# Kernel optimization log

Hardware: AMD Instinct MI355X
Metric: run time of the kernel (lower is better)

## Reference

```python
import jax, jax.numpy as jnp
import numpy as np

N = 200000
E = 3200000


def _init_linear(key, fan_in, fan_out):
    kw, kb = jax.random.split(key)
    bound = 1.0 / np.sqrt(fan_in)
    W = jax.random.uniform(kw, (fan_in, fan_out), jnp.float32, -bound, bound)
    b = jax.random.uniform(kb, (fan_out,), jnp.float32, -bound, bound)
    return W, b


def setup_inputs() -> dict:
    key = jax.random.key(0)
    ks = jax.random.split(key, 8)
    latent_features = jax.random.normal(ks[0], (N, 256), jnp.float32)
    history = jax.random.uniform(ks[1], (N,), jnp.float32)
    is_subgoal = jax.random.uniform(ks[2], (N,), jnp.float32)
    edge_index = jax.random.randint(ks[3], (2, E), 0, N, dtype=jnp.int64)
    W1, b1 = _init_linear(ks[4], 258, 128)
    W2, b2 = _init_linear(ks[5], 128, 64)
    W3, b3 = _init_linear(ks[6], 64, 8)
    Wc, bc = _init_linear(ks[7], 8, 3)
    return {"latent_features": latent_features, "history": history,
            "is_subgoal": is_subgoal, "edge_index": edge_index,
            "W1": W1, "b1": b1, "W2": W2, "b2": b2,
            "W3": W3, "b3": b3, "Wc": Wc, "bc": bc}


def _gcn_conv(h, W, b, src, dst, norm, n):
    # PyG GCNConv: linear transform, then symmetric-normalized scatter-add.
    h = h @ W                                  # [n, F_out]
    msg = norm[:, None] * h[src]               # gather + edge-norm, [E+n, F_out]
    out = jax.ops.segment_sum(msg, dst, num_segments=n)
    return out + b


def reference(latent_features, history, is_subgoal, edge_index,
              W1, b1, W2, b2, W3, b3, Wc, bc):
    n = latent_features.shape[0]
    # add self-loops (GCNConv default add_self_loops=True)
    loop = jnp.arange(n, dtype=edge_index.dtype)
    src = jnp.concatenate([edge_index[0], loop])
    dst = jnp.concatenate([edge_index[1], loop])
    # symmetric normalization: deg over destination (incl. self-loops)
    deg = jax.ops.segment_sum(jnp.ones_like(dst, dtype=jnp.float32), dst,
                              num_segments=n)
    dinv = jnp.where(deg > 0, jax.lax.rsqrt(deg), 0.0)
    norm = dinv[src] * dinv[dst]               # [E+n]

    h = jnp.concatenate([latent_features, history[:, None],
                         is_subgoal[:, None]], axis=1)  # [n, 258]
    h = jax.nn.relu(_gcn_conv(h, W1, b1, src, dst, norm, n))
    h = jax.nn.relu(_gcn_conv(h, W2, b2, src, dst, norm, n))
    h = jax.nn.relu(_gcn_conv(h, W3, b3, src, dst, norm, n))
    return h @ Wc + bc                          # [n, 3]
```

## Files before the change

### kernel.cpp

```cpp
#include <hip/hip_runtime.h>
#include <hip/hip_fp16.h>


#define N_NODES 200000
#define N_EDGES 3200000
#define NBUCK 782

static_assert(N_NODES % 64 == 0, "tiling");
static_assert((NBUCK - 1) * 256 < N_NODES && NBUCK * 256 >= N_NODES, "buckets");

typedef unsigned int u32;
typedef _Float16 f16;
typedef __attribute__((ext_vector_type(8))) _Float16 f16x8;
typedef __attribute__((ext_vector_type(4))) _Float16 f16x4;
typedef __attribute__((ext_vector_type(4))) float f32x4;
typedef __attribute__((ext_vector_type(2))) float f32x2;


__global__ __launch_bounds__(256) void k_bhist(const int* __restrict__ dst,
                                               int* __restrict__ bcnt) {
    __shared__ int lh[NBUCK];
    int t = threadIdx.x;
    for (int b = t; b < NBUCK; b += 256) lh[b] = 0;
    __syncthreads();
    long e0 = (long)blockIdx.x * 8192;
    for (int k = 0; k < 32; ++k) {
        long e = e0 + k * 256 + t;
        if (e < N_EDGES) atomicAdd(&lh[dst[e] >> 8], 1);
    }
    __syncthreads();
    for (int b = t; b < NBUCK; b += 256)
        if (lh[b]) atomicAdd(&bcnt[b], lh[b]);
}


__global__ __launch_bounds__(256) void k_bscan(const int* __restrict__ bcnt,
                                               int* __restrict__ boff,
                                               int* __restrict__ bcur,
                                               int* __restrict__ row) {
    __shared__ int sm[256];
    int t = threadIdx.x;
    int base = t * 4;
    int a0 = (base + 0 < NBUCK) ? bcnt[base + 0] : 0;
    int a1 = (base + 1 < NBUCK) ? bcnt[base + 1] : 0;
    int a2 = (base + 2 < NBUCK) ? bcnt[base + 2] : 0;
    int a3 = (base + 3 < NBUCK) ? bcnt[base + 3] : 0;
    int s = a0 + a1 + a2 + a3;
    sm[t] = s;
    __syncthreads();
    for (int o = 1; o < 256; o <<= 1) {
        int v = (t >= o) ? sm[t - o] : 0;
        __syncthreads();
        sm[t] += v;
        __syncthreads();
    }
    int excl = sm[t] - s;
    if (base + 0 < NBUCK) { boff[base + 0] = excl;               bcur[base + 0] = excl; }
    if (base + 1 < NBUCK) { boff[base + 1] = excl + a0;          bcur[base + 1] = excl + a0; }
    if (base + 2 < NBUCK) { boff[base + 2] = excl + a0 + a1;     bcur[base + 2] = excl + a0 + a1; }
    if (base + 3 < NBUCK) { boff[base + 3] = excl + a0 + a1 + a2; bcur[base + 3] = excl + a0 + a1 + a2; }
    if (t == 255) { boff[NBUCK] = N_EDGES; row[N_NODES] = N_EDGES; }
}


__global__ __launch_bounds__(256) void k_scatter(const int* __restrict__ src,
                                                 const int* __restrict__ dst,
                                                 int* __restrict__ bcur,
                                                 u32* __restrict__ entries) {
    __shared__ int lh[NBUCK];
    __shared__ int base[NBUCK];
    __shared__ int lcur[NBUCK];
    int t = threadIdx.x;
    for (int b = t; b < NBUCK; b += 256) lh[b] = 0;
    __syncthreads();
    long e0 = (long)blockIdx.x * 8192;
    for (int k = 0; k < 32; ++k) {
        long e = e0 + k * 256 + t;
        if (e < N_EDGES) atomicAdd(&lh[dst[e] >> 8], 1);
    }
    __syncthreads();
    for (int b = t; b < NBUCK; b += 256) {
        base[b] = atomicAdd(&bcur[b], lh[b]);
        lcur[b] = 0;
    }
    __syncthreads();
    for (int k = 0; k < 32; ++k) {
        long e = e0 + k * 256 + t;
        if (e < N_EDGES) {
            int d = dst[e];
            int bkt = d >> 8;
            int p = base[bkt] + atomicAdd(&lcur[bkt], 1);
            entries[p] = ((u32)src[e] << 8) | (u32)(d & 255);
        }
    }
}


__global__ __launch_bounds__(256) void k_prep(const u32* __restrict__ entries,
                                              const int* __restrict__ boff,
                                              int* __restrict__ row,
                                              float* __restrict__ dinv,
                                              int* __restrict__ col) {
    __shared__ int lh[256];
    __shared__ int sc[256];
    __shared__ int cur[256];
    const int b = blockIdx.x, t = threadIdx.x;
    const int s = boff[b], e = boff[b + 1];
    const int cnt = e - s;
    lh[t] = 0;
    __syncthreads();
    for (int i = t; i < cnt; i += 256) atomicAdd(&lh[entries[s + i] & 255], 1);
    __syncthreads();
    int my = lh[t];
    sc[t] = my;
    __syncthreads();
    for (int o = 1; o < 256; o <<= 1) {
        int v = (t >= o) ? sc[t - o] : 0;
        __syncthreads();
        sc[t] += v;
        __syncthreads();
    }
    int excl = sc[t] - my;
    int node = b * 256 + t;
    if (node < N_NODES) {
        row[node] = s + excl;
        dinv[node] = rsqrtf((float)(my + 1));
    }
    cur[t] = s + excl;
    __syncthreads();
    for (int i = t; i < cnt; i += 256) {
        u32 en = entries[s + i];
        int p = atomicAdd(&cur[en & 255], 1);
        col[p] = (int)(en >> 8);
    }
}


__global__ __launch_bounds__(256) void k_prepw(const float* __restrict__ W,
                                               f16* __restrict__ Wth,
                                               f16* __restrict__ Wtl) {
    int t = blockIdx.x * 256 + threadIdx.x;
    int k = t >> 7;
    int f = t & 127;
    float w = W[k * 128 + f];
    f16 hi = (f16)w;
    f16 lo = (f16)(w - (float)hi);
    Wth[f * 256 + k] = hi;
    Wtl[f * 256 + k] = lo;
}


__global__ __launch_bounds__(256) void k_prepw2(const float* __restrict__ W2,
                                                f16* __restrict__ Wh,
                                                f16* __restrict__ Wl) {
    int t = blockIdx.x * 256 + threadIdx.x;
    int k = t >> 6;
    int f = t & 63;
    float w = W2[k * 64 + f];
    f16 hi = (f16)w;
    Wh[f * 128 + k] = hi;
    Wl[f * 128 + k] = (f16)(w - (float)hi);
}


__global__ __launch_bounds__(1024) void k_gemm1(const float* __restrict__ X,
                                                const float* __restrict__ hist,
                                                const float* __restrict__ subg,
                                                const float* __restrict__ W,
                                                const f16* __restrict__ Wth,
                                                const f16* __restrict__ Wtl,
                                                const float* __restrict__ dinv,
                                                __half2* __restrict__ g1) {
    __shared__ f16 Ws[2][128 * 256];
    const int t = threadIdx.x;

    {
        const int r = t >> 3;
        const int seg = t & 7;
        const f16* gh = Wth + r * 256 + seg * 32;
        const f16* gl = Wtl + r * 256 + seg * 32;
        const int sw = (r & 7) << 4;
        const int base = r * 512 + seg * 64;
        char* wsh = (char*)&Ws[0][0];
        char* wsl = (char*)&Ws[1][0];
#pragma unroll
        for (int q = 0; q < 4; ++q) {
            *(f16x8*)(wsh + ((base + q * 16) ^ sw)) = *(const f16x8*)(gh + q * 8);
            *(f16x8*)(wsl + ((base + q * 16) ^ sw)) = *(const f16x8*)(gl + q * 8);
        }
    }

    const int wv = t >> 6;
    const int l = t & 63;
    const int l15 = l & 15;
    const int lk = l >> 4;
    const int nb = blockIdx.x * 256;
    const int node = nb + wv * 16 + l15;
    const int xrow = node < N_NODES ? node : N_NODES - 1;
    const float* xbase = X + (size_t)xrow * 256 + lk * 8;

    f32x4 acc[8];
#pragma unroll
    for (int fb = 0; fb < 8; ++fb) acc[fb] = (f32x4){0.f, 0.f, 0.f, 0.f};

    float4 pa = *(const float4*)(xbase + 0);
    float4 pb = *(const float4*)(xbase + 4);

    __syncthreads();

    const char* wsh = (const char*)&Ws[0][0];
    const char* wsl = (const char*)&Ws[1][0];
    const int sw = (l15 & 7) << 4;

    for (int kc = 0; kc < 256; kc += 32) {
        float xs[8] = {pa.x, pa.y, pa.z, pa.w, pb.x, pb.y, pb.z, pb.w};
        if (kc + 32 < 256) {
            pa = *(const float4*)(xbase + kc + 32);
            pb = *(const float4*)(xbase + kc + 36);
        }
        union { f16 h[8]; f16x8 v; } H, L;
#pragma unroll
        for (int i = 0; i < 8; ++i) {
            f16 h = (f16)xs[i];
            H.h[i] = h;
            L.h[i] = (f16)(xs[i] - (float)h);
        }
        f16x8 xh = H.v, xl = L.v;

        const int koff = ((kc + lk * 8) * 2) ^ sw;
#pragma unroll
        for (int fb = 0; fb < 8; ++fb) {
            const int off = (fb * 16 + l15) * 512 + koff;
            f16x8 wh = *(const f16x8*)(wsh + off);
            f16x8 wl = *(const f16x8*)(wsl + off);
            acc[fb] = __builtin_amdgcn_mfma_f32_16x16x32_f16(wh, xh, acc[fb], 0, 0, 0);
            acc[fb] = __builtin_amdgcn_mfma_f32_16x16x32_f16(wh, xl, acc[fb], 0, 0, 0);
            acc[fb] = __builtin_amdgcn_mfma_f32_16x16x32_f16(wl, xh, acc[fb], 0, 0, 0);
        }
    }

    const bool ok = node < N_NODES;
    const float hh = hist[xrow];
    const float ss = subg[xrow];
    const float dv = dinv[xrow];
    char* orow = (char*)g1 + (size_t)node * 256;
#pragma unroll
    for (int fb = 0; fb < 8; ++fb) {
        const int f0 = fb * 16 + lk * 4;
        float4 w6 = *(const float4*)(W + 256 * 128 + f0);
        float4 w7 = *(const float4*)(W + 257 * 128 + f0);
        union { f16 h[4]; float2 v; } o;
        o.h[0] = (f16)((acc[fb][0] + hh * w6.x + ss * w7.x) * dv);
        o.h[1] = (f16)((acc[fb][1] + hh * w6.y + ss * w7.y) * dv);
        o.h[2] = (f16)((acc[fb][2] + hh * w6.z + ss * w7.z) * dv);
        o.h[3] = (f16)((acc[fb][3] + hh * w6.w + ss * w7.w) * dv);
        if (ok) *(float2*)(orow + fb * 32 + lk * 8) = o.v;
    }
}


__global__ __launch_bounds__(1024) void k_ag2(const __half2* __restrict__ g,
                                              const int* __restrict__ row,
                                              const int* __restrict__ col,
                                              const float* __restrict__ dinv,
                                              const float* __restrict__ bias,
                                              const f16* __restrict__ W2hg,
                                              const f16* __restrict__ W2lg,
                                              __half2* __restrict__ g2) {
    __shared__ f16 Xh[64][136];
    __shared__ f16 Xl[64][136];
    __shared__ f16 Wh[64][136];
    __shared__ f16 Wl[64][136];
    const int t = threadIdx.x;
    const int nb = blockIdx.x * 64;

    {
        const int r = t >> 4;
        const int sg = (t & 15) * 8;
        *(f16x8*)&Wh[r][sg] = *(const f16x8*)(W2hg + r * 128 + sg);
        *(f16x8*)&Wl[r][sg] = *(const f16x8*)(W2lg + r * 128 + sg);
    }

    const int wv = t >> 6;
    const int l = t & 63;
    const int hf = l >> 5;
    const int ln = l & 31;
    const f16x4* gp = (const f16x4*)g;
    const float4 b4 = *(const float4*)(bias + ln * 4);
    for (int i = 0; i < 2; ++i) {
        const int nloc = wv * 4 + hf * 2 + i;
        const int node = nb + nloc;
        f32x4 a = (f32x4){0.f, 0.f, 0.f, 0.f};
        const int s = row[node];
        const int e = row[node + 1];
        int idx = s;
        for (; idx + 8 <= e; idx += 8) {
            u32 off[8];
            f16x4 h[8];
#pragma unroll
            for (int u = 0; u < 8; ++u) off[u] = ((u32)col[idx + u] << 5) + ln;
#pragma unroll
            for (int u = 0; u < 8; ++u) h[u] = gp[off[u]];
#pragma unroll
            for (int u = 0; u < 8; ++u) a += __builtin_convertvector(h[u], f32x4);
        }
        for (; idx < e; ++idx)
            a += __builtin_convertvector(gp[((u32)col[idx] << 5) + ln], f32x4);
        f32x4 fs = __builtin_convertvector(gp[((u32)node << 5) + ln], f32x4);
        const float di = dinv[node];
        float v0 = fmaxf(di * (a[0] + fs[0]) + b4.x, 0.f);
        float v1 = fmaxf(di * (a[1] + fs[1]) + b4.y, 0.f);
        float v2 = fmaxf(di * (a[2] + fs[2]) + b4.z, 0.f);
        float v3 = fmaxf(di * (a[3] + fs[3]) + b4.w, 0.f);
        f16 h0 = (f16)v0, h1 = (f16)v1, h2 = (f16)v2, h3 = (f16)v3;
        f16x4 hi = {h0, h1, h2, h3};
        f16x4 lo = {(f16)(v0 - (float)h0), (f16)(v1 - (float)h1),
                    (f16)(v2 - (float)h2), (f16)(v3 - (float)h3)};
        *(f16x4*)&Xh[nloc][ln * 4] = hi;
        *(f16x4*)&Xl[nloc][ln * 4] = lo;
    }
    __syncthreads();

    const int l15 = l & 15;
    const int lk = l >> 4;
    const int nw = wv & 3;
    const int fw = wv >> 2;
    f32x4 acc = (f32x4){0.f, 0.f, 0.f, 0.f};
#pragma unroll
    for (int kc = 0; kc < 128; kc += 32) {
        f16x8 xh = *(const f16x8*)&Xh[nw * 16 + l15][kc + lk * 8];
        f16x8 xl = *(const f16x8*)&Xl[nw * 16 + l15][kc + lk * 8];
        f16x8 wh = *(const f16x8*)&Wh[fw * 16 + l15][kc + lk * 8];
        f16x8 wl = *(const f16x8*)&Wl[fw * 16 + l15][kc + lk * 8];
        acc = __builtin_amdgcn_mfma_f32_16x16x32_f16(wh, xh, acc, 0, 0, 0);
        acc = __builtin_amdgcn_mfma_f32_16x16x32_f16(wh, xl, acc, 0, 0, 0);
        acc = __builtin_amdgcn_mfma_f32_16x16x32_f16(wl, xh, acc, 0, 0, 0);
    }
    const int node = nb + nw * 16 + l15;
    const float dv = dinv[node];
    union { f16 h[4]; float2 v; } o;
#pragma unroll
    for (int r = 0; r < 4; ++r) o.h[r] = (f16)(acc[r] * dv);
    *(float2*)((char*)g2 + (size_t)node * 128 + fw * 32 + lk * 8) = o.v;
}


__global__ __launch_bounds__(256) void k_ag3(const __half2* __restrict__ g,
                                             const int* __restrict__ row,
                                             const int* __restrict__ col,
                                             const float* __restrict__ dinv,
                                             const float* __restrict__ bias,
                                             const float* __restrict__ W3,
                                             float* __restrict__ g3) {
    __shared__ float h3s[32][68];
    __shared__ float W3t[8][68];
    const int t = threadIdx.x;
    const int nb = blockIdx.x * 32;

    for (int i = t; i < 512; i += 256) {
        int k = i & 63, f = i >> 6;
        W3t[f][k] = W3[k * 8 + f];
    }

    const int wv = t >> 6;
    const int l = t & 63;
    const int q = l >> 4;
    const int ln = l & 15;
    const f16x4* gp = (const f16x4*)g;
    const float4 b4 = *(const float4*)(bias + ln * 4);
    for (int i = 0; i < 2; ++i) {
        const int nloc = wv * 8 + q * 2 + i;
        const int node = nb + nloc;
        f32x4 a = (f32x4){0.f, 0.f, 0.f, 0.f};
        const int s = row[node];
        const int e = row[node + 1];
        int idx = s;
        for (; idx + 8 <= e; idx += 8) {
            u32 off[8];
            f16x4 h[8];
#pragma unroll
            for (int u = 0; u < 8; ++u) off[u] = ((u32)col[idx + u] << 4) + ln;
#pragma unroll
            for (int u = 0; u < 8; ++u) h[u] = gp[off[u]];
#pragma unroll
            for (int u = 0; u < 8; ++u) a += __builtin_convertvector(h[u], f32x4);
        }
        for (; idx < e; ++idx)
            a += __builtin_convertvector(gp[((u32)col[idx] << 4) + ln], f32x4);
        f32x4 fs = __builtin_convertvector(gp[((u32)node << 4) + ln], f32x4);
        const float di = dinv[node];
        float4 o;
        o.x = fmaxf(di * (a[0] + fs[0]) + b4.x, 0.f);
        o.y = fmaxf(di * (a[1] + fs[1]) + b4.y, 0.f);
        o.z = fmaxf(di * (a[2] + fs[2]) + b4.z, 0.f);
        o.w = fmaxf(di * (a[3] + fs[3]) + b4.w, 0.f);
        *(float4*)&h3s[nloc][ln * 4] = o;
    }
    __syncthreads();

    const int node = t >> 3;
    const int f = t & 7;
    float acc = 0.f;
#pragma unroll
    for (int k4 = 0; k4 < 16; ++k4) {
        float4 x = *(const float4*)&h3s[node][k4 * 4];
        float4 w = *(const float4*)&W3t[f][k4 * 4];
        acc += x.x * w.x + x.y * w.y + x.z * w.z + x.w * w.w;
    }
    g3[(size_t)(nb + node) * 8 + f] = dinv[nb + node] * acc;
}


__global__ __launch_bounds__(256) void k_agf(const float* __restrict__ g,
                                             const int* __restrict__ row,
                                             const int* __restrict__ col,
                                             const float* __restrict__ dinv,
                                             const float* __restrict__ bias,
                                             const float* __restrict__ Wc,
                                             const float* __restrict__ bc,
                                             float* __restrict__ out) {
    __shared__ float h4s[64][10];
    __shared__ float Wcs[24];
    __shared__ float bcs[3];
    const int t = threadIdx.x;
    const int nb = blockIdx.x * 64;
    if (t < 24) Wcs[t] = Wc[t];
    if (t < 3) bcs[t] = bc[t];

    const int node = t >> 2;
    const int c = t & 3;
    const f32x2* gp = (const f32x2*)g;
    const float2 b2 = *(const float2*)(bias + c * 2);
    f32x2 a = (f32x2){0.f, 0.f};
    const int s = row[nb + node];
    const int e = row[nb + node + 1];
    int idx = s;
    for (; idx + 8 <= e; idx += 8) {
        u32 off[8];
        f32x2 v[8];
#pragma unroll
        for (int u = 0; u < 8; ++u) off[u] = ((u32)col[idx + u] << 2) + c;
#pragma unroll
        for (int u = 0; u < 8; ++u) v[u] = gp[off[u]];
#pragma unroll
        for (int u = 0; u < 8; ++u) a += v[u];
    }
    for (; idx < e; ++idx) a += gp[((u32)col[idx] << 2) + c];
    a += gp[((u32)(nb + node) << 2) + c];
    const float di = dinv[nb + node];
    float2 o;
    o.x = fmaxf(di * a[0] + b2.x, 0.f);
    o.y = fmaxf(di * a[1] + b2.y, 0.f);
    *(float2*)&h4s[node][c * 2] = o;
    __syncthreads();

    if ((t & 3) < 3) {
        const int n2 = t >> 2;
        const int cc = t & 3;
        float o2 = bcs[cc];
#pragma unroll
        for (int k = 0; k < 8; ++k) o2 += h4s[n2][k] * Wcs[k * 3 + cc];
        out[(size_t)(nb + n2) * 3 + cc] = o2;
    }
}


extern "C" void kernel_launch(void* const* d_in, const int* in_sizes, int n_in,
                              void* d_out, int out_size, void* d_ws, size_t ws_size,
                              hipStream_t stream) {
    const float* latent = (const float*)d_in[0];
    const float* hist = (const float*)d_in[1];
    const float* subg = (const float*)d_in[2];
    const int* eidx = (const int*)d_in[3];
    const float* W1 = (const float*)d_in[4];
    const float* b1 = (const float*)d_in[5];
    const float* W2 = (const float*)d_in[6];
    const float* b2 = (const float*)d_in[7];
    const float* W3 = (const float*)d_in[8];
    const float* b3 = (const float*)d_in[9];
    const float* Wc = (const float*)d_in[10];
    const float* bc = (const float*)d_in[11];
    float* outp = (float*)d_out;

    char* ws = (char*)d_ws;
    size_t off = 0;
    auto take = [&](size_t bytes) -> void* {
        void* p = ws + off;
        off += (bytes + 255) & ~(size_t)255;
        return p;
    };
    float* dinv = (float*)take((size_t)N_NODES * 4);
    int* row = (int*)take((size_t)(N_NODES + 1) * 4);
    int* col = (int*)take((size_t)N_EDGES * 4);
    u32* entries = (u32*)take((size_t)N_EDGES * 4);
    int* bcnt = (int*)take((size_t)NBUCK * 4);
    int* boff = (int*)take((size_t)(NBUCK + 1) * 4);
    int* bcur = (int*)take((size_t)NBUCK * 4);
    __half2* bufH = (__half2*)take((size_t)N_NODES * 128 * 2);
    __half2* bufG2 = (__half2*)take((size_t)N_NODES * 64 * 2);
    float* bufG3 = (float*)take((size_t)N_NODES * 8 * 4);
    f16* Wth = (f16*)take((size_t)128 * 256 * 2);
    f16* Wtl = (f16*)take((size_t)128 * 256 * 2);
    f16* W2h = (f16*)take((size_t)64 * 128 * 2);
    f16* W2l = (f16*)take((size_t)64 * 128 * 2);

    const int* srcp = eidx;
    const int* dstp = eidx + N_EDGES;

    const int scat_blocks = (N_EDGES + 8191) / 8192;

    hipMemsetAsync(bcnt, 0, (size_t)NBUCK * 4, stream);
    k_prepw<<<128, 256, 0, stream>>>(W1, Wth, Wtl);
    k_prepw2<<<32, 256, 0, stream>>>(W2, W2h, W2l);
    k_bhist<<<scat_blocks, 256, 0, stream>>>(dstp, bcnt);
    k_bscan<<<1, 256, 0, stream>>>(bcnt, boff, bcur, row);
    k_scatter<<<scat_blocks, 256, 0, stream>>>(srcp, dstp, bcur, entries);
    k_prep<<<NBUCK, 256, 0, stream>>>(entries, boff, row, dinv, col);

    k_gemm1<<<(N_NODES + 255) / 256, 1024, 0, stream>>>(latent, hist, subg, W1, Wth, Wtl, dinv, bufH);
    k_ag2<<<N_NODES / 64, 1024, 0, stream>>>(bufH, row, col, dinv, b1, W2h, W2l, bufG2);
    k_ag3<<<N_NODES / 32, 256, 0, stream>>>(bufG2, row, col, dinv, b2, W3, bufG3);
    k_agf<<<N_NODES / 64, 256, 0, stream>>>(bufG3, row, col, dinv, b3, Wc, bc, outp);
}
```

Measured before the change: 727.4 us.

## Replace bucket count/scan with fixed-capacity buckets and interleave two-node gathers

Drops the bucket histogram and scan kernels by giving each destination bucket a fixed slab of BCAP entries, with per-node start/end arrays replacing the CSR row pointer. The aggregation kernels for layers two and three now gather neighbors of two nodes in an interleaved loop to expose more outstanding loads, and the final aggregation gets a deeper unroll. This removes a full pass over dst and two launches. In exchange it assumes no bucket exceeds BCAP, clamping writes (and corrupting results) if one does.

```diff
diff --git a/kernel.cpp b/kernel.cpp
--- a/kernel.cpp
+++ b/kernel.cpp
@@ -5,6 +5,7 @@
 #define N_NODES 200000
 #define N_EDGES 3200000
 #define NBUCK 782
+#define BCAP 5120
 
 static_assert(N_NODES % 64 == 0, "tiling");
 static_assert((NBUCK - 1) * 256 < N_NODES && NBUCK * 256 >= N_NODES, "buckets");
@@ -15,52 +16,6 @@
 typedef __attribute__((ext_vector_type(4))) _Float16 f16x4;
 typedef __attribute__((ext_vector_type(4))) float f32x4;
 typedef __attribute__((ext_vector_type(2))) float f32x2;
-
-
-__global__ __launch_bounds__(256) void k_bhist(const int* __restrict__ dst,
-                                               int* __restrict__ bcnt) {
-    __shared__ int lh[NBUCK];
-    int t = threadIdx.x;
-    for (int b = t; b < NBUCK; b += 256) lh[b] = 0;
-    __syncthreads();
-    long e0 = (long)blockIdx.x * 8192;
-    for (int k = 0; k < 32; ++k) {
-        long e = e0 + k * 256 + t;
-        if (e < N_EDGES) atomicAdd(&lh[dst[e] >> 8], 1);
-    }
-    __syncthreads();
-    for (int b = t; b < NBUCK; b += 256)
-        if (lh[b]) atomicAdd(&bcnt[b], lh[b]);
-}
-
-
-__global__ __launch_bounds__(256) void k_bscan(const int* __restrict__ bcnt,
-                                               int* __restrict__ boff,
-                                               int* __restrict__ bcur,
-                                               int* __restrict__ row) {
-    __shared__ int sm[256];
-    int t = threadIdx.x;
-    int base = t * 4;
-    int a0 = (base + 0 < NBUCK) ? bcnt[base + 0] : 0;
-    int a1 = (base + 1 < NBUCK) ? bcnt[base + 1] : 0;
-    int a2 = (base + 2 < NBUCK) ? bcnt[base + 2] : 0;
-    int a3 = (base + 3 < NBUCK) ? bcnt[base + 3] : 0;
-    int s = a0 + a1 + a2 + a3;
-    sm[t] = s;
-    __syncthreads();
-    for (int o = 1; o < 256; o <<= 1) {
-        int v = (t >= o) ? sm[t - o] : 0;
-        __syncthreads();
-        sm[t] += v;
-        __syncthreads();
-    }
-    int excl = sm[t] - s;
-    if (base + 0 < NBUCK) { boff[base + 0] = excl;               bcur[base + 0] = excl; }
-    if (base + 1 < NBUCK) { boff[base + 1] = excl + a0;          bcur[base + 1] = excl + a0; }
-    if (base + 2 < NBUCK) { boff[base + 2] = excl + a0 + a1;     bcur[base + 2] = excl + a0 + a1; }
-    if (base + 3 < NBUCK) { boff[base + 3] = excl + a0 + a1 + a2; bcur[base + 3] = excl + a0 + a1 + a2; }
-    if (t == 255) { boff[NBUCK] = N_EDGES; row[N_NODES] = N_EDGES; }
-}
 
 
 __global__ __launch_bounds__(256) void k_scatter(const int* __restrict__ src,
@@ -80,7 +35,7 @@
     }
     __syncthreads();
     for (int b = t; b < NBUCK; b += 256) {
-        base[b] = atomicAdd(&bcur[b], lh[b]);
+        base[b] = lh[b] ? atomicAdd(&bcur[b], lh[b]) : 0;
         lcur[b] = 0;
     }
     __syncthreads();
@@ -90,26 +45,29 @@
             int d = dst[e];
             int bkt = d >> 8;
             int p = base[bkt] + atomicAdd(&lcur[bkt], 1);
-            entries[p] = ((u32)src[e] << 8) | (u32)(d & 255);
+            p = p < BCAP ? p : BCAP - 1;
+            entries[(size_t)bkt * BCAP + p] = ((u32)src[e] << 8) | (u32)(d & 255);
         }
     }
 }
 
 
 __global__ __launch_bounds__(256) void k_prep(const u32* __restrict__ entries,
-                                              const int* __restrict__ boff,
-                                              int* __restrict__ row,
+                                              const int* __restrict__ bcur,
+                                              int* __restrict__ rs,
+                                              int* __restrict__ re,
                                               float* __restrict__ dinv,
                                               int* __restrict__ col) {
     __shared__ int lh[256];
     __shared__ int sc[256];
     __shared__ int cur[256];
     const int b = blockIdx.x, t = threadIdx.x;
-    const int s = boff[b], e = boff[b + 1];
-    const int cnt = e - s;
+    int cnt = bcur[b];
+    cnt = cnt < BCAP ? cnt : BCAP;
+    const u32* ent = entries + (size_t)b * BCAP;
     lh[t] = 0;
     __syncthreads();
-    for (int i = t; i < cnt; i += 256) atomicAdd(&lh[entries[s + i] & 255], 1);
+    for (int i = t; i < cnt; i += 256) atomicAdd(&lh[ent[i] & 255], 1);
     __syncthreads();
     int my = lh[t];
     sc[t] = my;
@@ -123,13 +81,14 @@
     int excl = sc[t] - my;
     int node = b * 256 + t;
     if (node < N_NODES) {
-        row[node] = s + excl;
+        rs[node] = b * BCAP + excl;
+        re[node] = b * BCAP + excl + my;
         dinv[node] = rsqrtf((float)(my + 1));
     }
-    cur[t] = s + excl;
+    cur[t] = b * BCAP + excl;
     __syncthreads();
     for (int i = t; i < cnt; i += 256) {
-        u32 en = entries[s + i];
+        u32 en = ent[i];
         int p = atomicAdd(&cur[en & 255], 1);
         col[p] = (int)(en >> 8);
     }
@@ -260,7 +219,8 @@
 
 
 __global__ __launch_bounds__(1024) void k_ag2(const __half2* __restrict__ g,
-                                              const int* __restrict__ row,
+                                              const int* __restrict__ rs,
+                                              const int* __restrict__ re,
                                               const int* __restrict__ col,
                                               const float* __restrict__ dinv,
                                               const float* __restrict__ bias,
@@ -287,25 +247,57 @@
     const int ln = l & 31;
     const f16x4* gp = (const f16x4*)g;
     const float4 b4 = *(const float4*)(bias + ln * 4);
+    const int n0 = nb + wv * 4 + hf * 2;
+    const int n1 = n0 + 1;
+    f32x4 a0 = (f32x4){0.f, 0.f, 0.f, 0.f};
+    f32x4 a1 = (f32x4){0.f, 0.f, 0.f, 0.f};
+    int i0 = rs[n0], e0i = re[n0];
+    int i1 = rs[n1], e1i = re[n1];
+    while (i0 + 8 <= e0i && i1 + 8 <= e1i) {
+        u32 offA[8], offB[8];
+        f16x4 hA[8], hB[8];
+#pragma unroll
+        for (int u = 0; u < 8; ++u) offA[u] = ((u32)col[i0 + u] << 5) + ln;
+#pragma unroll
+        for (int u = 0; u < 8; ++u) offB[u] = ((u32)col[i1 + u] << 5) + ln;
+#pragma unroll
+        for (int u = 0; u < 8; ++u) hA[u] = gp[offA[u]];
+#pragma unroll
+        for (int u = 0; u < 8; ++u) hB[u] = gp[offB[u]];
+#pragma unroll
+        for (int u = 0; u < 8; ++u) a0 += __builtin_convertvector(hA[u], f32x4);
+#pragma unroll
+        for (int u = 0; u < 8; ++u) a1 += __builtin_convertvector(hB[u], f32x4);
+        i0 += 8;
+        i1 += 8;
+    }
+    for (; i0 + 8 <= e0i; i0 += 8) {
+        u32 off[8];
+        f16x4 h[8];
+#pragma unroll
+        for (int u = 0; u < 8; ++u) off[u] = ((u32)col[i0 + u] << 5) + ln;
+#pragma unroll
+        for (int u = 0; u < 8; ++u) h[u] = gp[off[u]];
+#pragma unroll
+        for (int u = 0; u < 8; ++u) a0 += __builtin_convertvector(h[u], f32x4);
+    }
+    for (; i1 + 8 <= e1i; i1 += 8) {
+        u32 off[8];
+        f16x4 h[8];
+#pragma unroll
+        for (int u = 0; u < 8; ++u) off[u] = ((u32)col[i1 + u] << 5) + ln;
+#pragma unroll
+        for (int u = 0; u < 8; ++u) h[u] = gp[off[u]];
+#pragma unroll
+        for (int u = 0; u < 8; ++u) a1 += __builtin_convertvector(h[u], f32x4);
+    }
+    for (; i0 < e0i; ++i0) a0 += __builtin_convertvector(gp[((u32)col[i0] << 5) + ln], f32x4);
+    for (; i1 < e1i; ++i1) a1 += __builtin_convertvector(gp[((u32)col[i1] << 5) + ln], f32x4);
+
+#pragma unroll
     for (int i = 0; i < 2; ++i) {
-        const int nloc = wv * 4 + hf * 2 + i;
-        const int node = nb + nloc;
-        f32x4 a = (f32x4){0.f, 0.f, 0.f, 0.f};
-        const int s = row[node];
-        const int e = row[node + 1];
-        int idx = s;
-        for (; idx + 8 <= e; idx += 8) {
-            u32 off[8];
-            f16x4 h[8];
-#pragma unroll
-            for (int u = 0; u < 8; ++u) off[u] = ((u32)col[idx + u] << 5) + ln;
-#pragma unroll
-            for (int u = 0; u < 8; ++u) h[u] = gp[off[u]];
-#pragma unroll
-            for (int u = 0; u < 8; ++u) a += __builtin_convertvector(h[u], f32x4);
-        }
-        for (; idx < e; ++idx)
-            a += __builtin_convertvector(gp[((u32)col[idx] << 5) + ln], f32x4);
+        const int node = i ? n1 : n0;
+        f32x4 a = i ? a1 : a0;
         f32x4 fs = __builtin_convertvector(gp[((u32)node << 5) + ln], f32x4);
         const float di = dinv[node];
         float v0 = fmaxf(di * (a[0] + fs[0]) + b4.x, 0.f);
@@ -316,8 +308,8 @@
         f16x4 hi = {h0, h1, h2, h3};
         f16x4 lo = {(f16)(v0 - (float)h0), (f16)(v1 - (float)h1),
                     (f16)(v2 - (float)h2), (f16)(v3 - (float)h3)};
-        *(f16x4*)&Xh[nloc][ln * 4] = hi;
-        *(f16x4*)&Xl[nloc][ln * 4] = lo;
+        *(f16x4*)&Xh[node - nb][ln * 4] = hi;
+        *(f16x4*)&Xl[node - nb][ln * 4] = lo;
     }
     __syncthreads();
 
@@ -346,7 +338,8 @@
 
 
 __global__ __launch_bounds__(256) void k_ag3(const __half2* __restrict__ g,
-                                             const int* __restrict__ row,
+                                             const int* __restrict__ rs,
+                                             const int* __restrict__ re,
                                              const int* __restrict__ col,
                                              const float* __restrict__ dinv,
                                              const float* __restrict__ bias,
@@ -368,25 +361,57 @@
     const int ln = l & 15;
     const f16x4* gp = (const f16x4*)g;
     const float4 b4 = *(const float4*)(bias + ln * 4);
+    const int n0 = nb + wv * 8 + q * 2;
+    const int n1 = n0 + 1;
+    f32x4 a0 = (f32x4){0.f, 0.f, 0.f, 0.f};
+    f32x4 a1 = (f32x4){0.f, 0.f, 0.f, 0.f};
+    int i0 = rs[n0], e0i = re[n0];
+    int i1 = rs[n1], e1i = re[n1];
+    while (i0 + 8 <= e0i && i1 + 8 <= e1i) {
+        u32 offA[8], offB[8];
+        f16x4 hA[8], hB[8];
+#pragma unroll
+        for (int u = 0; u < 8; ++u) offA[u] = ((u32)col[i0 + u] << 4) + ln;
+#pragma unroll
+        for (int u = 0; u < 8; ++u) offB[u] = ((u32)col[i1 + u] << 4) + ln;
+#pragma unroll
+        for (int u = 0; u < 8; ++u) hA[u] = gp[offA[u]];
+#pragma unroll
+        for (int u = 0; u < 8; ++u) hB[u] = gp[offB[u]];
+#pragma unroll
+        for (int u = 0; u < 8; ++u) a0 += __builtin_convertvector(hA[u], f32x4);
+#pragma unroll
+        for (int u = 0; u < 8; ++u) a1 += __builtin_convertvector(hB[u], f32x4);
+        i0 += 8;
+        i1 += 8;
+    }
+    for (; i0 + 8 <= e0i; i0 += 8) {
+        u32 off[8];
+        f16x4 h[8];
+#pragma unroll
+        for (int u = 0; u < 8; ++u) off[u] = ((u32)col[i0 + u] << 4) + ln;
+#pragma unroll
+        for (int u = 0; u < 8; ++u) h[u] = gp[off[u]];
+#pragma unroll
+        for (int u = 0; u < 8; ++u) a0 += __builtin_convertvector(h[u], f32x4);
+    }
+    for (; i1 + 8 <= e1i; i1 += 8) {
+        u32 off[8];
+        f16x4 h[8];
+#pragma unroll
+        for (int u = 0; u < 8; ++u) off[u] = ((u32)col[i1 + u] << 4) + ln;
+#pragma unroll
+        for (int u = 0; u < 8; ++u) h[u] = gp[off[u]];
+#pragma unroll
+        for (int u = 0; u < 8; ++u) a1 += __builtin_convertvector(h[u], f32x4);
+    }
+    for (; i0 < e0i; ++i0) a0 += __builtin_convertvector(gp[((u32)col[i0] << 4) + ln], f32x4);
+    for (; i1 < e1i; ++i1) a1 += __builtin_convertvector(gp[((u32)col[i1] << 4) + ln], f32x4);
+
+#pragma unroll
     for (int i = 0; i < 2; ++i) {
-        const int nloc = wv * 8 + q * 2 + i;
-        const int node = nb + nloc;
-        f32x4 a = (f32x4){0.f, 0.f, 0.f, 0.f};
-        const int s = row[node];
-        const int e = row[node + 1];
-        int idx = s;
-        for (; idx + 8 <= e; idx += 8) {
-            u32 off[8];
-            f16x4 h[8];
-#pragma unroll
-            for (int u = 0; u < 8; ++u) off[u] = ((u32)col[idx + u] << 4) + ln;
-#pragma unroll
-            for (int u = 0; u < 8; ++u) h[u] = gp[off[u]];
-#pragma unroll
-            for (int u = 0; u < 8; ++u) a += __builtin_convertvector(h[u], f32x4);
-        }
-        for (; idx < e; ++idx)
-            a += __builtin_convertvector(gp[((u32)col[idx] << 4) + ln], f32x4);
+        const int node = i ? n1 : n0;
+        f32x4 a = i ? a1 : a0;
         f32x4 fs = __builtin_convertvector(gp[((u32)node << 4) + ln], f32x4);
         const float di = dinv[node];
         float4 o;
@@ -394,7 +419,7 @@
         o.y = fmaxf(di * (a[1] + fs[1]) + b4.y, 0.f);
         o.z = fmaxf(di * (a[2] + fs[2]) + b4.z, 0.f);
         o.w = fmaxf(di * (a[3] + fs[3]) + b4.w, 0.f);
-        *(float4*)&h3s[nloc][ln * 4] = o;
+        *(float4*)&h3s[node - nb][ln * 4] = o;
     }
     __syncthreads();
 
@@ -412,7 +437,8 @@
 
 
 __global__ __launch_bounds__(256) void k_agf(const float* __restrict__ g,
-                                             const int* __restrict__ row,
+                                             const int* __restrict__ rs,
+                                             const int* __restrict__ re,
                                              const int* __restrict__ col,
                                              const float* __restrict__ dinv,
                                              const float* __restrict__ bias,
@@ -432,9 +458,19 @@
     const f32x2* gp = (const f32x2*)g;
     const float2 b2 = *(const float2*)(bias + c * 2);
     f32x2 a = (f32x2){0.f, 0.f};
-    const int s = row[nb + node];
-    const int e = row[nb + node + 1];
+    const int s = rs[nb + node];
+    const int e = re[nb + node];
     int idx = s;
+    for (; idx + 16 <= e; idx += 16) {
+        u32 off[16];
+        f32x2 v[16];
+#pragma unroll
+        for (int u = 0; u < 16; ++u) off[u] = ((u32)col[idx + u] << 2) + c;
+#pragma unroll
+        for (int u = 0; u < 16; ++u) v[u] = gp[off[u]];
+#pragma unroll
+        for (int u = 0; u < 16; ++u) a += v[u];
+    }
     for (; idx + 8 <= e; idx += 8) {
         u32 off[8];
         f32x2 v[8];
@@ -490,11 +526,10 @@
         return p;
     };
     float* dinv = (float*)take((size_t)N_NODES * 4);
-    int* row = (int*)take((size_t)(N_NODES + 1) * 4);
-    int* col = (int*)take((size_t)N_EDGES * 4);
-    u32* entries = (u32*)take((size_t)N_EDGES * 4);
-    int* bcnt = (int*)take((size_t)NBUCK * 4);
-    int* boff = (int*)take((size_t)(NBUCK + 1) * 4);
+    int* rs = (int*)take((size_t)N_NODES * 4);
+    int* re = (int*)take((size_t)N_NODES * 4);
+    int* col = (int*)take((size_t)NBUCK * BCAP * 4);
+    u32* entries = (u32*)take((size_t)NBUCK * BCAP * 4);
     int* bcur = (int*)take((size_t)NBUCK * 4);
     __half2* bufH = (__half2*)take((size_t)N_NODES * 128 * 2);
     __half2* bufG2 = (__half2*)take((size_t)N_NODES * 64 * 2);
@@ -509,16 +544,14 @@
 
     const int scat_blocks = (N_EDGES + 8191) / 8192;
 
-    hipMemsetAsync(bcnt, 0, (size_t)NBUCK * 4, stream);
+    hipMemsetAsync(bcur, 0, (size_t)NBUCK * 4, stream);
     k_prepw<<<128, 256, 0, stream>>>(W1, Wth, Wtl);
     k_prepw2<<<32, 256, 0, stream>>>(W2, W2h, W2l);
-    k_bhist<<<scat_blocks, 256, 0, stream>>>(dstp, bcnt);
-    k_bscan<<<1, 256, 0, stream>>>(bcnt, boff, bcur, row);
     k_scatter<<<scat_blocks, 256, 0, stream>>>(srcp, dstp, bcur, entries);
-    k_prep<<<NBUCK, 256, 0, stream>>>(entries, boff, row, dinv, col);
+    k_prep<<<NBUCK, 256, 0, stream>>>(entries, bcur, rs, re, dinv, col);
 
     k_gemm1<<<(N_NODES + 255) / 256, 1024, 0, stream>>>(latent, hist, subg, W1, Wth, Wtl, dinv, bufH);
-    k_ag2<<<N_NODES / 64, 1024, 0, stream>>>(bufH, row, col, dinv, b1, W2h, W2l, bufG2);
-    k_ag3<<<N_NODES / 32, 256, 0, stream>>>(bufG2, row, col, dinv, b2, W3, bufG3);
-    k_agf<<<N_NODES / 64, 256, 0, stream>>>(bufG3, row, col, dinv, b3, Wc, bc, outp);
-}
+    k_ag2<<<N_NODES / 64, 1024, 0, stream>>>(bufH, rs, re, col, dinv, b1, W2h, W2l, bufG2);
+    k_ag3<<<N_NODES / 32, 256, 0, stream>>>(bufG2, rs, re, col, dinv, b2, W3, bufG3);
+    k_agf<<<N_NODES / 64, 256, 0, stream>>>(bufG3, rs, re, col, dinv, b3, Wc, bc, outp);
+}
```

After: 790.5 us. 1.09x slower.
